# Kernel optimization log

Hardware: AMD Instinct MI355X
Metric: run time of the kernel (lower is better)

The kernel has to match this reference:

```python
import jax, jax.numpy as jnp
import numpy as np

EPS = 1e-5
B, N, K = 2, 40960, 16
D_OUT = 64
H = D_OUT // 2  # 32

PNAMES = ['mlp1_w','mlp1_b','mlp1_g','mlp1_beta','mlp1_m','mlp1_v',
          'ap1_fc_w','ap1_fc_b','ap1_mlp_w','ap1_mlp_b','ap1_g','ap1_beta','ap1_m','ap1_v',
          'mlp2_w','mlp2_b','mlp2_g','mlp2_beta','mlp2_m','mlp2_v',
          'ap2_fc_w','ap2_fc_b','ap2_mlp_w','ap2_mlp_b','ap2_g','ap2_beta','ap2_m','ap2_v']


def _conv1x1(x, w, b):
    # x: (B,C,N,K), w: (O,C) -> (B,O,N,K)
    return jnp.einsum('oc,bcnk->bonk', w, x) + b[None, :, None, None]


def _bn(x, g, beta, m, v):
    # eval-mode BatchNorm2d over channel axis 1
    scale = g / jnp.sqrt(v + EPS)
    return (x - m[None, :, None, None]) * scale[None, :, None, None] + beta[None, :, None, None]


def _gather_neighbour(pc, idx):
    # pc: (B,N,d), idx: (B,N,K) -> (B,N,K,d)
    b, n, d = pc.shape
    k = idx.shape[-1]
    flat = idx.reshape(b, n * k)
    feats = jnp.take_along_axis(pc, flat[:, :, None], axis=1)  # (B,N*K,d)
    return feats.reshape(b, n, k, d)


def _rel_pos_enc(xyz, idx):
    nbr = _gather_neighbour(xyz, idx)                       # (B,N,K,3)
    tile = jnp.broadcast_to(xyz[:, :, None, :], nbr.shape)  # (B,N,K,3)
    rel = tile - nbr
    dist = jnp.sqrt(jnp.sum(rel * rel, axis=-1, keepdims=True))
    return jnp.concatenate([dist, rel, tile, nbr], axis=-1)  # (B,N,K,10)


def _att_pool(f, fc_w, fc_b, mw, mb, g, beta, m, v):
    # f: (B,C,N,K)
    att = jax.nn.relu(_conv1x1(f, fc_w, fc_b))
    scores = jax.nn.softmax(att, axis=3)
    agg = jnp.sum(f * scores, axis=3, keepdims=True)        # (B,C,N,1)
    return jax.nn.relu(_bn(_conv1x1(agg, mw, mb), g, beta, m, v))


def _forward(xyz, feature, neigh_idx, p):
    # relative pos encoding -> (B,10,N,K)
    f_xyz = _rel_pos_enc(xyz, neigh_idx).transpose(0, 3, 1, 2)
    f_xyz = jax.nn.relu(_bn(_conv1x1(f_xyz, p['mlp1_w'], p['mlp1_b']),
                            p['mlp1_g'], p['mlp1_beta'], p['mlp1_m'], p['mlp1_v']))  # (B,H,N,K)
    f_nb = _gather_neighbour(feature[..., 0].transpose(0, 2, 1), neigh_idx).transpose(0, 3, 1, 2)  # (B,H,N,K)
    f_cat = jnp.concatenate([f_nb, f_xyz], axis=1)          # (B,D_OUT,N,K)
    f_agg = _att_pool(f_cat, p['ap1_fc_w'], p['ap1_fc_b'], p['ap1_mlp_w'], p['ap1_mlp_b'],
                      p['ap1_g'], p['ap1_beta'], p['ap1_m'], p['ap1_v'])  # (B,H,N,1)
    f_xyz = jax.nn.relu(_bn(_conv1x1(f_xyz, p['mlp2_w'], p['mlp2_b']),
                            p['mlp2_g'], p['mlp2_beta'], p['mlp2_m'], p['mlp2_v']))  # (B,H,N,K)
    f_nb = _gather_neighbour(f_agg[..., 0].transpose(0, 2, 1), neigh_idx).transpose(0, 3, 1, 2)  # (B,H,N,K)
    f_cat = jnp.concatenate([f_nb, f_xyz], axis=1)          # (B,D_OUT,N,K)
    return _att_pool(f_cat, p['ap2_fc_w'], p['ap2_fc_b'], p['ap2_mlp_w'], p['ap2_mlp_b'],
                     p['ap2_g'], p['ap2_beta'], p['ap2_m'], p['ap2_v'])  # (B,D_OUT,N,1)


def setup_inputs() -> dict:
    key = jax.random.key(0)
    ks = iter(jax.random.split(key, 64))

    def w(o, c):
        return jax.random.normal(next(ks), (o, c), jnp.float32) * float(np.sqrt(2.0 / c))

    def bias(c):
        return jax.random.normal(next(ks), (c,), jnp.float32) * 0.01

    def bnp(c):
        g = jax.random.uniform(next(ks), (c,), jnp.float32, 0.5, 1.5)
        beta = jax.random.normal(next(ks), (c,), jnp.float32) * 0.1
        m = jax.random.normal(next(ks), (c,), jnp.float32) * 0.1
        v = jax.random.uniform(next(ks), (c,), jnp.float32, 0.5, 1.5)
        return g, beta, m, v

    inp = {}
    inp['xyz'] = jax.random.normal(next(ks), (B, N, 3), jnp.float32)
    inp['feature'] = jax.random.normal(next(ks), (B, H, N, 1), jnp.float32)
    inp['mlp1_w'], inp['mlp1_b'] = w(H, 10), bias(H)
    inp['mlp1_g'], inp['mlp1_beta'], inp['mlp1_m'], inp['mlp1_v'] = bnp(H)
    inp['ap1_fc_w'], inp['ap1_fc_b'] = w(D_OUT, D_OUT), bias(D_OUT)
    inp['ap1_mlp_w'], inp['ap1_mlp_b'] = w(H, D_OUT), bias(H)
    inp['ap1_g'], inp['ap1_beta'], inp['ap1_m'], inp['ap1_v'] = bnp(H)
    inp['mlp2_w'], inp['mlp2_b'] = w(H, H), bias(H)
    inp['mlp2_g'], inp['mlp2_beta'], inp['mlp2_m'], inp['mlp2_v'] = bnp(H)
    inp['ap2_fc_w'], inp['ap2_fc_b'] = w(D_OUT, D_OUT), bias(D_OUT)
    inp['ap2_mlp_w'], inp['ap2_mlp_b'] = w(D_OUT, D_OUT), bias(D_OUT)
    inp['ap2_g'], inp['ap2_beta'], inp['ap2_m'], inp['ap2_v'] = bnp(D_OUT)
    inp['neigh_idx'] = jax.random.randint(next(ks), (B, N, K), 0, N, jnp.int64 if jax.config.jax_enable_x64 else jnp.int32)
    return inp


def reference(xyz, feature, mlp1_w, mlp1_b, mlp1_g, mlp1_beta, mlp1_m, mlp1_v,
              ap1_fc_w, ap1_fc_b, ap1_mlp_w, ap1_mlp_b, ap1_g, ap1_beta, ap1_m, ap1_v,
              mlp2_w, mlp2_b, mlp2_g, mlp2_beta, mlp2_m, mlp2_v,
              ap2_fc_w, ap2_fc_b, ap2_mlp_w, ap2_mlp_b, ap2_g, ap2_beta, ap2_m, ap2_v,
              neigh_idx):
    p = dict(zip(PNAMES, (mlp1_w, mlp1_b, mlp1_g, mlp1_beta, mlp1_m, mlp1_v,
                          ap1_fc_w, ap1_fc_b, ap1_mlp_w, ap1_mlp_b, ap1_g, ap1_beta, ap1_m, ap1_v,
                          mlp2_w, mlp2_b, mlp2_g, mlp2_beta, mlp2_m, mlp2_v,
                          ap2_fc_w, ap2_fc_b, ap2_mlp_w, ap2_mlp_b, ap2_g, ap2_beta, ap2_m, ap2_v)))
    return _forward(xyz, feature, neigh_idx, p)
```

## Files before the change

### kernel.cpp

```cpp
#include <hip/hip_runtime.h>
#include <math.h>

#define BB 2
#define NN 40960
#define KK 16

typedef float v2f __attribute__((ext_vector_type(2)));
__device__ __forceinline__ v2f fma2(v2f a, v2f b, v2f c){
  return __builtin_elementwise_fma(a, b, c);
}

template<int CTRL>
__device__ __forceinline__ float dppf(float x){
  return __int_as_float(__builtin_amdgcn_update_dpp(0, __float_as_int(x), CTRL, 0xF, 0xF, true));
}
__device__ __forceinline__ float red16_sum(float v){
  v += dppf<0xB1>(v);
  v += dppf<0x4E>(v);
  v += dppf<0x141>(v);
  v += dppf<0x140>(v);
  return v;
}

__device__ alignas(16) float g_pw1[32*10];
__device__ alignas(16) float g_pb1[32];
__device__ alignas(16) float g_pw2[32*32];
__device__ alignas(16) float g_pb2[32];
__device__ alignas(16) float g_pcw[32*64];
__device__ alignas(16) float g_pcb[32];
__device__ alignas(16) float g_pdw[64*64];
__device__ alignas(16) float g_pdb[64];

__global__ __launch_bounds__(256) void k_pre(
  const float* __restrict__ feat, float* __restrict__ feat_t,
  const float* __restrict__ w1, const float* __restrict__ b1,
  const float* __restrict__ g1, const float* __restrict__ be1, const float* __restrict__ m1, const float* __restrict__ v1,
  const float* __restrict__ w2, const float* __restrict__ b2,
  const float* __restrict__ g2, const float* __restrict__ be2, const float* __restrict__ m2, const float* __restrict__ v2,
  const float* __restrict__ cw, const float* __restrict__ cb,
  const float* __restrict__ cg, const float* __restrict__ cbe, const float* __restrict__ cm, const float* __restrict__ cv,
  const float* __restrict__ dw, const float* __restrict__ db,
  const float* __restrict__ dg, const float* __restrict__ dbe, const float* __restrict__ dm, const float* __restrict__ dv)
{
  int tid = threadIdx.x;
  int bid = blockIdx.x;
  if (bid < BB*NN/256){
    int b = bid / (NN/256);
    int n = (bid % (NN/256))*256 + tid;
    float v[32];
    #pragma unroll
    for (int h=0; h<32; ++h) v[h] = feat[((size_t)(b*32+h))*NN + n];
    float* o = feat_t + ((size_t)b*NN + n)*32;
    #pragma unroll
    for (int h=0; h<32; h+=4){ *(float4*)(o+h) = make_float4(v[h],v[h+1],v[h+2],v[h+3]); }
    return;
  }
  for (int i=tid; i<320; i+=256){ int h=i/10;
    g_pw1[i] = w1[i] * (g1[h]*rsqrtf(v1[h]+1e-5f)); }
  if (tid<32){ float s=g1[tid]*rsqrtf(v1[tid]+1e-5f);
    g_pb1[tid] = (b1[tid]-m1[tid])*s + be1[tid]; }
  for (int i=tid; i<1024; i+=256){ int h=i>>5;
    g_pw2[i] = w2[i] * (g2[h]*rsqrtf(v2[h]+1e-5f)); }
  if (tid<32){ float s=g2[tid]*rsqrtf(v2[tid]+1e-5f);
    g_pb2[tid] = (b2[tid]-m2[tid])*s + be2[tid]; }
  for (int i=tid; i<2048; i+=256){ int h=i>>6;
    g_pcw[i] = cw[i] * (cg[h]*rsqrtf(cv[h]+1e-5f)); }
  if (tid<32){ float s=cg[tid]*rsqrtf(cv[tid]+1e-5f);
    g_pcb[tid] = (cb[tid]-cm[tid])*s + cbe[tid]; }
  for (int i=tid; i<4096; i+=256){ int h=i>>6;
    g_pdw[i] = dw[i] * (dg[h]*rsqrtf(dv[h]+1e-5f)); }
  if (tid<64){ float s=dg[tid]*rsqrtf(dv[tid]+1e-5f);
    g_pdb[tid] = (db[tid]-dm[tid])*s + dbe[tid]; }
}

__global__ __launch_bounds__(256,2) void k_stage1(
  const float* __restrict__ xyz, const float* __restrict__ feat_t, const int* __restrict__ nidx,
  const float* __restrict__ fcw, const float* __restrict__ fcb,
  float* __restrict__ fagg)
{
  int tid = threadIdx.x;
  int lane = tid & 63, wvv = tid >> 6;
  int k = lane & 15, ns = lane >> 4;
  int b = blockIdx.x / (NN/16);
  int n = (blockIdx.x % (NN/16))*16 + wvv*4 + ns;
  size_t bn = (size_t)b*NN + n;
  int idxv = nidx[bn*KK + k];

  alignas(16) float fc_[64];
  const float* fb = feat_t + ((size_t)b*NN + idxv)*32;
  #pragma unroll
  for (int h=0; h<32; h+=4){ float4 x=*(const float4*)(fb+h);
    fc_[h]=x.x; fc_[h+1]=x.y; fc_[h+2]=x.z; fc_[h+3]=x.w; }

  const float* tp = xyz + bn*3;
  const float* qp = xyz + ((size_t)b*NN + idxv)*3;
  float t0=tp[0],t1=tp[1],t2=tp[2];
  float q0=qp[0],q1=qp[1],q2=qp[2];
  float r0=t0-q0,r1=t1-q1,r2=t2-q2;
  v2f e2[5] = { {sqrtf(r0*r0+r1*r1+r2*r2), r0}, {r1,r2}, {t0,t1}, {t2,q0}, {q1,q2} };

  #pragma unroll
  for (int h=0; h<32; ++h){
    const v2f* wr = (const v2f*)(g_pw1 + h*10);
    v2f acc = {g_pb1[h], 0.f};
    #pragma unroll
    for (int c=0; c<5; ++c) acc = fma2(wr[c], e2[c], acc);
    fc_[32+h] = fmaxf(acc.x+acc.y, 0.f);
  }

  const v2f* fv = (const v2f*)fc_;
  float sp4[4], sf4[4];
  #pragma unroll
  for (int ob=0; ob<64; ob+=2){
    const v2f* w0 = (const v2f*)(fcw + ob*64);
    const v2f* w1 = (const v2f*)(fcw + (ob+1)*64);
    v2f acc0 = {fcb[ob], 0.f}, acc1 = {fcb[ob+1], 0.f};
    #pragma unroll
    for (int c=0; c<32; ++c){ acc0 = fma2(w0[c], fv[c], acc0); acc1 = fma2(w1[c], fv[c], acc1); }
    float a0 = fmaxf(acc0.x+acc0.y, 0.f), a1 = fmaxf(acc1.x+acc1.y, 0.f);
    float p0 = __expf(a0), p1 = __expf(a1);
    float g0 = fc_[ob]*p0,  g1v = fc_[ob+1]*p1;
    float sp0 = red16_sum(p0), sf0 = red16_sum(g0);
    float sp1 = red16_sum(p1), sf1 = red16_sum(g1v);
    if ((ob>>2)==k){ sp4[ob&3]=sp0; sf4[ob&3]=sf0; sp4[(ob+1)&3]=sp1; sf4[(ob+1)&3]=sf1; }
  }
  v2f a01, a23;
  a01.x=__fdividef(sf4[0],sp4[0]); a01.y=__fdividef(sf4[1],sp4[1]);
  a23.x=__fdividef(sf4[2],sp4[2]); a23.y=__fdividef(sf4[3],sp4[3]);

  float o0=0.f, o1=0.f;
  #pragma unroll
  for (int h=0; h<32; ++h){
    const v2f* wr = (const v2f*)(g_pcw + h*64 + 4*k);
    v2f p2 = fma2(wr[0], a01, wr[1]*a23);
    float part = red16_sum(p2.x + p2.y);
    float val = fmaxf(part + g_pcb[h], 0.f);
    if ((h&15)==k){ if (h<16) o0=val; else o1=val; }
  }
  float* fo = fagg + bn*32;
  fo[k]=o0; fo[k+16]=o1;
}

__global__ __launch_bounds__(256,2) void k_stage2(
  const float* __restrict__ xyz, const float* __restrict__ fagg, const int* __restrict__ nidx,
  const float* __restrict__ fcw, const float* __restrict__ fcb,
  float* __restrict__ outp)
{
  int tid = threadIdx.x;
  int lane = tid & 63, wvv = tid >> 6;
  int k = lane & 15, ns = lane >> 4;
  int b = blockIdx.x / (NN/16);
  int n = (blockIdx.x % (NN/16))*16 + wvv*4 + ns;
  size_t bn = (size_t)b*NN + n;
  int idxv = nidx[bn*KK + k];

  alignas(16) float fc_[64];
  const float* fb = fagg + ((size_t)b*NN + idxv)*32;
  #pragma unroll
  for (int h=0; h<32; h+=4){ float4 x=*(const float4*)(fb+h);
    fc_[h]=x.x; fc_[h+1]=x.y; fc_[h+2]=x.z; fc_[h+3]=x.w; }

  const float* tp = xyz + bn*3;
  const float* qp = xyz + ((size_t)b*NN + idxv)*3;
  float t0=tp[0],t1=tp[1],t2=tp[2];
  float q0=qp[0],q1=qp[1],q2=qp[2];
  float r0=t0-q0,r1=t1-q1,r2=t2-q2;
  v2f e2[5] = { {sqrtf(r0*r0+r1*r1+r2*r2), r0}, {r1,r2}, {t0,t1}, {t2,q0}, {q1,q2} };

  alignas(8) float fx[32];
  #pragma unroll
  for (int h=0; h<32; ++h){
    const v2f* wr = (const v2f*)(g_pw1 + h*10);
    v2f acc = {g_pb1[h], 0.f};
    #pragma unroll
    for (int c=0; c<5; ++c) acc = fma2(wr[c], e2[c], acc);
    fx[h] = fmaxf(acc.x+acc.y, 0.f);
  }

  const v2f* fxv = (const v2f*)fx;
  #pragma unroll
  for (int h=0; h<32; ++h){
    const v2f* wr = (const v2f*)(g_pw2 + h*32);
    v2f acc = {g_pb2[h], 0.f};
    #pragma unroll
    for (int c=0; c<16; ++c) acc = fma2(wr[c], fxv[c], acc);
    fc_[32+h] = fmaxf(acc.x+acc.y, 0.f);
  }

  const v2f* fv = (const v2f*)fc_;
  float sp4[4], sf4[4];
  #pragma unroll
  for (int ob=0; ob<64; ob+=2){
    const v2f* w0 = (const v2f*)(fcw + ob*64);
    const v2f* w1 = (const v2f*)(fcw + (ob+1)*64);
    v2f acc0 = {fcb[ob], 0.f}, acc1 = {fcb[ob+1], 0.f};
    #pragma unroll
    for (int c=0; c<32; ++c){ acc0 = fma2(w0[c], fv[c], acc0); acc1 = fma2(w1[c], fv[c], acc1); }
    float a0 = fmaxf(acc0.x+acc0.y, 0.f), a1 = fmaxf(acc1.x+acc1.y, 0.f);
    float p0 = __expf(a0), p1 = __expf(a1);
    float g0 = fc_[ob]*p0,  g1v = fc_[ob+1]*p1;
    float sp0 = red16_sum(p0), sf0 = red16_sum(g0);
    float sp1 = red16_sum(p1), sf1 = red16_sum(g1v);
    if ((ob>>2)==k){ sp4[ob&3]=sp0; sf4[ob&3]=sf0; sp4[(ob+1)&3]=sp1; sf4[(ob+1)&3]=sf1; }
  }
  v2f a01, a23;
  a01.x=__fdividef(sf4[0],sp4[0]); a01.y=__fdividef(sf4[1],sp4[1]);
  a23.x=__fdividef(sf4[2],sp4[2]); a23.y=__fdividef(sf4[3],sp4[3]);

  float o4[4];
  #pragma unroll
  for (int h=0; h<64; ++h){
    const v2f* wr = (const v2f*)(g_pdw + h*64 + 4*k);
    v2f p2 = fma2(wr[0], a01, wr[1]*a23);
    float part = red16_sum(p2.x + p2.y);
    float val = fmaxf(part + g_pdb[h], 0.f);
    if ((h&15)==k) o4[h>>4] = val;
  }
  #pragma unroll
  for (int j=0; j<4; ++j)
    outp[((size_t)(b*64 + k + 16*j))*NN + n] = o4[j];
}

extern "C" void kernel_launch(void* const* d_in, const int* in_sizes, int n_in,
                              void* d_out, int out_size, void* d_ws, size_t ws_size,
                              hipStream_t stream){
  const float* xyz     = (const float*)d_in[0];
  const float* feature = (const float*)d_in[1];
  const int*   nidx    = (const int*)d_in[30];
  float* feat_t = (float*)d_ws;
  float* fagg   = feat_t + (size_t)BB*NN*32;

  k_pre<<<BB*NN/256 + 1, 256, 0, stream>>>(feature, feat_t,
    (const float*)d_in[2],(const float*)d_in[3],(const float*)d_in[4],(const float*)d_in[5],
    (const float*)d_in[6],(const float*)d_in[7],
    (const float*)d_in[16],(const float*)d_in[17],(const float*)d_in[18],(const float*)d_in[19],
    (const float*)d_in[20],(const float*)d_in[21],
    (const float*)d_in[10],(const float*)d_in[11],(const float*)d_in[12],(const float*)d_in[13],
    (const float*)d_in[14],(const float*)d_in[15],
    (const float*)d_in[24],(const float*)d_in[25],(const float*)d_in[26],(const float*)d_in[27],
    (const float*)d_in[28],(const float*)d_in[29]);
  k_stage1<<<BB*NN/16, 256, 0, stream>>>(xyz, feat_t, nidx,
    (const float*)d_in[8],(const float*)d_in[9], fagg);
  k_stage2<<<BB*NN/16, 256, 0, stream>>>(xyz, fagg, nidx,
    (const float*)d_in[22],(const float*)d_in[23], (float*)d_out);
}
```

Measured before the change: 453.3 us.

## Restructure stages so each wave loops over points with register-resident weights and LDS staging

Each wave now handles 16 points sequentially. Lane-indexed output channels keep the attention FC weights in registers, and the concatenated neighbour features are staged in LDS. This replaces the per-lane full 64x64 matvec and DPP reductions with an outer-product-style reuse across the 16 neighbours. Stage2 buffers its outputs in LDS so it can write coalesced float4 rows, and the grid shrinks to a quarter of the blocks with launch bounds raised to 3. The risks are higher register pressure from the 64-float weight arrays, serialised per-point latency inside each wave, and dependence on wave-level LDS ordering without a full barrier.

```diff
diff --git a/kernel.cpp b/kernel.cpp
--- a/kernel.cpp
+++ b/kernel.cpp
@@ -6,20 +6,14 @@
 #define KK 16
 
 typedef float v2f __attribute__((ext_vector_type(2)));
+__device__ __forceinline__ v2f mk2(float a, float b){ v2f r; r.x=a; r.y=b; return r; }
 __device__ __forceinline__ v2f fma2(v2f a, v2f b, v2f c){
   return __builtin_elementwise_fma(a, b, c);
 }
 
-template<int CTRL>
-__device__ __forceinline__ float dppf(float x){
-  return __int_as_float(__builtin_amdgcn_update_dpp(0, __float_as_int(x), CTRL, 0xF, 0xF, true));
-}
-__device__ __forceinline__ float red16_sum(float v){
-  v += dppf<0xB1>(v);
-  v += dppf<0x4E>(v);
-  v += dppf<0x141>(v);
-  v += dppf<0x140>(v);
-  return v;
+__device__ __forceinline__ void wave_sync(){
+  asm volatile("s_waitcnt lgkmcnt(0)" ::: "memory");
+  __builtin_amdgcn_sched_barrier(0);
 }
 
 __device__ alignas(16) float g_pw1[32*10];
@@ -73,152 +67,238 @@
     g_pdb[tid] = (db[tid]-dm[tid])*s + dbe[tid]; }
 }
 
-__global__ __launch_bounds__(256,2) void k_stage1(
+
+__global__ __launch_bounds__(256,3) void k_stage1(
   const float* __restrict__ xyz, const float* __restrict__ feat_t, const int* __restrict__ nidx,
   const float* __restrict__ fcw, const float* __restrict__ fcb,
   float* __restrict__ fagg)
 {
-  int tid = threadIdx.x;
-  int lane = tid & 63, wvv = tid >> 6;
-  int k = lane & 15, ns = lane >> 4;
-  int b = blockIdx.x / (NN/16);
-  int n = (blockIdx.x % (NN/16))*16 + wvv*4 + ns;
-  size_t bn = (size_t)b*NN + n;
-  int idxv = nidx[bn*KK + k];
-
-  alignas(16) float fc_[64];
-  const float* fb = feat_t + ((size_t)b*NN + idxv)*32;
-  #pragma unroll
-  for (int h=0; h<32; h+=4){ float4 x=*(const float4*)(fb+h);
-    fc_[h]=x.x; fc_[h+1]=x.y; fc_[h+2]=x.z; fc_[h+3]=x.w; }
-
-  const float* tp = xyz + bn*3;
-  const float* qp = xyz + ((size_t)b*NN + idxv)*3;
-  float t0=tp[0],t1=tp[1],t2=tp[2];
-  float q0=qp[0],q1=qp[1],q2=qp[2];
-  float r0=t0-q0,r1=t1-q1,r2=t2-q2;
-  v2f e2[5] = { {sqrtf(r0*r0+r1*r1+r2*r2), r0}, {r1,r2}, {t0,t1}, {t2,q0}, {q1,q2} };
-
-  #pragma unroll
-  for (int h=0; h<32; ++h){
-    const v2f* wr = (const v2f*)(g_pw1 + h*10);
-    v2f acc = {g_pb1[h], 0.f};
-    #pragma unroll
-    for (int c=0; c<5; ++c) acc = fma2(wr[c], e2[c], acc);
-    fc_[32+h] = fmaxf(acc.x+acc.y, 0.f);
-  }
-
-  const v2f* fv = (const v2f*)fc_;
-  float sp4[4], sf4[4];
-  #pragma unroll
-  for (int ob=0; ob<64; ob+=2){
-    const v2f* w0 = (const v2f*)(fcw + ob*64);
-    const v2f* w1 = (const v2f*)(fcw + (ob+1)*64);
-    v2f acc0 = {fcb[ob], 0.f}, acc1 = {fcb[ob+1], 0.f};
-    #pragma unroll
-    for (int c=0; c<32; ++c){ acc0 = fma2(w0[c], fv[c], acc0); acc1 = fma2(w1[c], fv[c], acc1); }
-    float a0 = fmaxf(acc0.x+acc0.y, 0.f), a1 = fmaxf(acc1.x+acc1.y, 0.f);
-    float p0 = __expf(a0), p1 = __expf(a1);
-    float g0 = fc_[ob]*p0,  g1v = fc_[ob+1]*p1;
-    float sp0 = red16_sum(p0), sf0 = red16_sum(g0);
-    float sp1 = red16_sum(p1), sf1 = red16_sum(g1v);
-    if ((ob>>2)==k){ sp4[ob&3]=sp0; sf4[ob&3]=sf0; sp4[(ob+1)&3]=sp1; sf4[(ob+1)&3]=sf1; }
-  }
-  v2f a01, a23;
-  a01.x=__fdividef(sf4[0],sp4[0]); a01.y=__fdividef(sf4[1],sp4[1]);
-  a23.x=__fdividef(sf4[2],sp4[2]); a23.y=__fdividef(sf4[3],sp4[3]);
-
-  float o0=0.f, o1=0.f;
-  #pragma unroll
-  for (int h=0; h<32; ++h){
-    const v2f* wr = (const v2f*)(g_pcw + h*64 + 4*k);
-    v2f p2 = fma2(wr[0], a01, wr[1]*a23);
-    float part = red16_sum(p2.x + p2.y);
-    float val = fmaxf(part + g_pcb[h], 0.f);
-    if ((h&15)==k){ if (h<16) o0=val; else o1=val; }
-  }
-  float* fo = fagg + bn*32;
-  fo[k]=o0; fo[k+16]=o1;
-}
-
-__global__ __launch_bounds__(256,2) void k_stage2(
+  __shared__ float s_fcat[4][16*68];
+  __shared__ float s_agg[4][64];
+  int tid = threadIdx.x, lane = tid&63, wvv = tid>>6;
+  int j = lane&15, cb = lane>>4;
+  int h_ap = lane&31, half = lane>>5;
+
+  float fcw_r[64];
+  {
+    const float4* src = (const float4*)(fcw + lane*64);
+    #pragma unroll
+    for (int c4=0;c4<16;++c4){ float4 w=src[c4];
+      fcw_r[4*c4]=w.x; fcw_r[4*c4+1]=w.y; fcw_r[4*c4+2]=w.z; fcw_r[4*c4+3]=w.w; }
+  }
+  float fcb_r = fcb[lane];
+  float pcw_r[32];
+  {
+    const float4* src = (const float4*)(g_pcw + h_ap*64 + half*32);
+    #pragma unroll
+    for (int c4=0;c4<8;++c4){ float4 w=src[c4];
+      pcw_r[4*c4]=w.x; pcw_r[4*c4+1]=w.y; pcw_r[4*c4+2]=w.z; pcw_r[4*c4+3]=w.w; }
+  }
+  float pcb_r = g_pcb[h_ap];
+
+  float* fcp = &s_fcat[wvv][0];
+  float* agp = &s_agg[wvv][0];
+  int pn0 = (blockIdx.x*4 + wvv)*16;
+  int b = (pn0 >= NN) ? 1 : 0;
+  int base = b*NN;
+
+  for (int t=0; t<16; ++t){
+    int pn = pn0 + t;
+    int idx = nidx[(size_t)pn*KK + j];
+    const float4* fbp = (const float4*)(feat_t + ((size_t)(base+idx))*32 + cb*8);
+    float4 g0 = fbp[0], g1 = fbp[1];
+
+    const float* tp = xyz + (size_t)pn*3;
+    const float* qp = xyz + (size_t)(base+idx)*3;
+    float t0=tp[0],t1=tp[1],t2=tp[2];
+    float q0=qp[0],q1=qp[1],q2=qp[2];
+    float r0=t0-q0,r1=t1-q1,r2=t2-q2;
+    v2f e2[5] = { {sqrtf(r0*r0+r1*r1+r2*r2),r0},{r1,r2},{t0,t1},{t2,q0},{q1,q2} };
+
+    float fx[32];
+    #pragma unroll
+    for (int h=0; h<32; ++h){
+      const v2f* wr = (const v2f*)(g_pw1 + h*10);
+      v2f a = mk2(g_pb1[h], 0.f);
+      #pragma unroll
+      for (int c=0;c<5;++c) a = fma2(wr[c], e2[c], a);
+      fx[h] = fmaxf(a.x+a.y, 0.f);
+    }
+    *(float4*)(fcp + j*68 + cb*8)     = g0;
+    *(float4*)(fcp + j*68 + cb*8 + 4) = g1;
+    if (lane < 16){
+      #pragma unroll
+      for (int c4=0;c4<8;++c4)
+        *(float4*)(fcp + j*68 + 32 + c4*4) =
+          make_float4(fx[4*c4],fx[4*c4+1],fx[4*c4+2],fx[4*c4+3]);
+    }
+    wave_sync();
+
+    float acc[16];
+    #pragma unroll
+    for (int j2=0;j2<16;++j2) acc[j2] = fcb_r;
+    #pragma unroll
+    for (int j2=0;j2<16;++j2){
+      const float4* fr = (const float4*)(fcp + j2*68);
+      #pragma unroll
+      for (int c4=0;c4<16;++c4){
+        float4 f = fr[c4];
+        acc[j2]=fmaf(fcw_r[4*c4+0],f.x,acc[j2]);
+        acc[j2]=fmaf(fcw_r[4*c4+1],f.y,acc[j2]);
+        acc[j2]=fmaf(fcw_r[4*c4+2],f.z,acc[j2]);
+        acc[j2]=fmaf(fcw_r[4*c4+3],f.w,acc[j2]);
+      }
+    }
+    float sp=0.f, sfp=0.f;
+    #pragma unroll
+    for (int j2=0;j2<16;++j2){ acc[j2] = __expf(fmaxf(acc[j2],0.f)); sp += acc[j2]; }
+    #pragma unroll
+    for (int j2=0;j2<16;++j2){ sfp = fmaf(fcp[j2*68 + lane], acc[j2], sfp); }
+    float aggv = __fdividef(sfp, sp);
+    agp[lane] = aggv;
+    wave_sync();
+
+    float part = 0.f;
+    const float4* ar = (const float4*)(agp + half*32);
+    #pragma unroll
+    for (int c4=0;c4<8;++c4){
+      float4 a = ar[c4];
+      part=fmaf(pcw_r[4*c4+0],a.x,part);
+      part=fmaf(pcw_r[4*c4+1],a.y,part);
+      part=fmaf(pcw_r[4*c4+2],a.z,part);
+      part=fmaf(pcw_r[4*c4+3],a.w,part);
+    }
+    part += __shfl_xor(part, 32);
+    float val = fmaxf(part + pcb_r, 0.f);
+    if (lane < 32) fagg[(size_t)pn*32 + lane] = val;
+    wave_sync();
+  }
+}
+
+__global__ __launch_bounds__(256,3) void k_stage2(
   const float* __restrict__ xyz, const float* __restrict__ fagg, const int* __restrict__ nidx,
   const float* __restrict__ fcw, const float* __restrict__ fcb,
   float* __restrict__ outp)
 {
-  int tid = threadIdx.x;
-  int lane = tid & 63, wvv = tid >> 6;
-  int k = lane & 15, ns = lane >> 4;
-  int b = blockIdx.x / (NN/16);
-  int n = (blockIdx.x % (NN/16))*16 + wvv*4 + ns;
-  size_t bn = (size_t)b*NN + n;
-  int idxv = nidx[bn*KK + k];
-
-  alignas(16) float fc_[64];
-  const float* fb = fagg + ((size_t)b*NN + idxv)*32;
+  __shared__ float s_fcat[4][16*68];
+  __shared__ float s_agg[4][64];
+  __shared__ float s_out[4][64*17];
+  __shared__ float s_w2[32*36];
+  int tid = threadIdx.x, lane = tid&63, wvv = tid>>6;
+  int j = lane&15, cb = lane>>4;
+
+  for (int i=tid; i<32*36; i+=256){ int h=i/36, c=i-h*36;
+    s_w2[i] = (c<32) ? g_pw2[h*32+c] : 0.f; }
+  __syncthreads();
+
+  float fcw_r[64];
+  {
+    const float4* src = (const float4*)(fcw + lane*64);
+    #pragma unroll
+    for (int c4=0;c4<16;++c4){ float4 w=src[c4];
+      fcw_r[4*c4]=w.x; fcw_r[4*c4+1]=w.y; fcw_r[4*c4+2]=w.z; fcw_r[4*c4+3]=w.w; }
+  }
+  float fcb_r = fcb[lane];
+  float pdb_r = g_pdb[lane];
+  float pb2_r[8];
   #pragma unroll
-  for (int h=0; h<32; h+=4){ float4 x=*(const float4*)(fb+h);
-    fc_[h]=x.x; fc_[h+1]=x.y; fc_[h+2]=x.z; fc_[h+3]=x.w; }
-
-  const float* tp = xyz + bn*3;
-  const float* qp = xyz + ((size_t)b*NN + idxv)*3;
-  float t0=tp[0],t1=tp[1],t2=tp[2];
-  float q0=qp[0],q1=qp[1],q2=qp[2];
-  float r0=t0-q0,r1=t1-q1,r2=t2-q2;
-  v2f e2[5] = { {sqrtf(r0*r0+r1*r1+r2*r2), r0}, {r1,r2}, {t0,t1}, {t2,q0}, {q1,q2} };
-
-  alignas(8) float fx[32];
-  #pragma unroll
-  for (int h=0; h<32; ++h){
-    const v2f* wr = (const v2f*)(g_pw1 + h*10);
-    v2f acc = {g_pb1[h], 0.f};
-    #pragma unroll
-    for (int c=0; c<5; ++c) acc = fma2(wr[c], e2[c], acc);
-    fx[h] = fmaxf(acc.x+acc.y, 0.f);
-  }
-
-  const v2f* fxv = (const v2f*)fx;
-  #pragma unroll
-  for (int h=0; h<32; ++h){
-    const v2f* wr = (const v2f*)(g_pw2 + h*32);
-    v2f acc = {g_pb2[h], 0.f};
-    #pragma unroll
-    for (int c=0; c<16; ++c) acc = fma2(wr[c], fxv[c], acc);
-    fc_[32+h] = fmaxf(acc.x+acc.y, 0.f);
-  }
-
-  const v2f* fv = (const v2f*)fc_;
-  float sp4[4], sf4[4];
-  #pragma unroll
-  for (int ob=0; ob<64; ob+=2){
-    const v2f* w0 = (const v2f*)(fcw + ob*64);
-    const v2f* w1 = (const v2f*)(fcw + (ob+1)*64);
-    v2f acc0 = {fcb[ob], 0.f}, acc1 = {fcb[ob+1], 0.f};
-    #pragma unroll
-    for (int c=0; c<32; ++c){ acc0 = fma2(w0[c], fv[c], acc0); acc1 = fma2(w1[c], fv[c], acc1); }
-    float a0 = fmaxf(acc0.x+acc0.y, 0.f), a1 = fmaxf(acc1.x+acc1.y, 0.f);
-    float p0 = __expf(a0), p1 = __expf(a1);
-    float g0 = fc_[ob]*p0,  g1v = fc_[ob+1]*p1;
-    float sp0 = red16_sum(p0), sf0 = red16_sum(g0);
-    float sp1 = red16_sum(p1), sf1 = red16_sum(g1v);
-    if ((ob>>2)==k){ sp4[ob&3]=sp0; sf4[ob&3]=sf0; sp4[(ob+1)&3]=sp1; sf4[(ob+1)&3]=sf1; }
-  }
-  v2f a01, a23;
-  a01.x=__fdividef(sf4[0],sp4[0]); a01.y=__fdividef(sf4[1],sp4[1]);
-  a23.x=__fdividef(sf4[2],sp4[2]); a23.y=__fdividef(sf4[3],sp4[3]);
-
-  float o4[4];
-  #pragma unroll
-  for (int h=0; h<64; ++h){
-    const v2f* wr = (const v2f*)(g_pdw + h*64 + 4*k);
-    v2f p2 = fma2(wr[0], a01, wr[1]*a23);
-    float part = red16_sum(p2.x + p2.y);
-    float val = fmaxf(part + g_pdb[h], 0.f);
-    if ((h&15)==k) o4[h>>4] = val;
-  }
-  #pragma unroll
-  for (int j=0; j<4; ++j)
-    outp[((size_t)(b*64 + k + 16*j))*NN + n] = o4[j];
+  for (int r=0;r<8;++r) pb2_r[r] = g_pb2[cb*8 + r];
+
+  float* fcp = &s_fcat[wvv][0];
+  float* agp = &s_agg[wvv][0];
+  float* sow = &s_out[wvv][0];
+  int pn0 = (blockIdx.x*4 + wvv)*16;
+  int b = (pn0 >= NN) ? 1 : 0;
+  int base = b*NN;
+
+  for (int t=0; t<16; ++t){
+    int pn = pn0 + t;
+    int idx = nidx[(size_t)pn*KK + j];
+    const float4* fbp = (const float4*)(fagg + ((size_t)(base+idx))*32 + cb*8);
+    float4 g0 = fbp[0], g1 = fbp[1];
+
+    const float* tp = xyz + (size_t)pn*3;
+    const float* qp = xyz + (size_t)(base+idx)*3;
+    float t0=tp[0],t1=tp[1],t2=tp[2];
+    float q0=qp[0],q1=qp[1],q2=qp[2];
+    float r0=t0-q0,r1=t1-q1,r2=t2-q2;
+    v2f e2[5] = { {sqrtf(r0*r0+r1*r1+r2*r2),r0},{r1,r2},{t0,t1},{t2,q0},{q1,q2} };
+
+    float fx[32];
+    #pragma unroll
+    for (int h=0; h<32; ++h){
+      const v2f* wr = (const v2f*)(g_pw1 + h*10);
+      v2f a = mk2(g_pb1[h], 0.f);
+      #pragma unroll
+      for (int c=0;c<5;++c) a = fma2(wr[c], e2[c], a);
+      fx[h] = fmaxf(a.x+a.y, 0.f);
+    }
+    float m8[8];
+    #pragma unroll
+    for (int r=0;r<8;++r){
+      const float4* wr = (const float4*)(s_w2 + (cb*8+r)*36);
+      float a = pb2_r[r];
+      #pragma unroll
+      for (int c4=0;c4<8;++c4){
+        float4 w = wr[c4];
+        a=fmaf(w.x,fx[4*c4+0],a); a=fmaf(w.y,fx[4*c4+1],a);
+        a=fmaf(w.z,fx[4*c4+2],a); a=fmaf(w.w,fx[4*c4+3],a);
+      }
+      m8[r] = fmaxf(a, 0.f);
+    }
+    *(float4*)(fcp + j*68 + cb*8)       = g0;
+    *(float4*)(fcp + j*68 + cb*8 + 4)   = g1;
+    *(float4*)(fcp + j*68 + 32 + cb*8)     = make_float4(m8[0],m8[1],m8[2],m8[3]);
+    *(float4*)(fcp + j*68 + 32 + cb*8 + 4) = make_float4(m8[4],m8[5],m8[6],m8[7]);
+    wave_sync();
+
+    float acc[16];
+    #pragma unroll
+    for (int j2=0;j2<16;++j2) acc[j2] = fcb_r;
+    #pragma unroll
+    for (int j2=0;j2<16;++j2){
+      const float4* fr = (const float4*)(fcp + j2*68);
+      #pragma unroll
+      for (int c4=0;c4<16;++c4){
+        float4 f = fr[c4];
+        acc[j2]=fmaf(fcw_r[4*c4+0],f.x,acc[j2]);
+        acc[j2]=fmaf(fcw_r[4*c4+1],f.y,acc[j2]);
+        acc[j2]=fmaf(fcw_r[4*c4+2],f.z,acc[j2]);
+        acc[j2]=fmaf(fcw_r[4*c4+3],f.w,acc[j2]);
+      }
+    }
+    float sp=0.f, sfp=0.f;
+    #pragma unroll
+    for (int j2=0;j2<16;++j2){ acc[j2] = __expf(fmaxf(acc[j2],0.f)); sp += acc[j2]; }
+    #pragma unroll
+    for (int j2=0;j2<16;++j2){ sfp = fmaf(fcp[j2*68 + lane], acc[j2], sfp); }
+    float aggv = __fdividef(sfp, sp);
+    agp[lane] = aggv;
+    wave_sync();
+
+    float part = 0.f;
+    const float4* wp = (const float4*)(g_pdw + lane*64);
+    const float4* ar = (const float4*)agp;
+    #pragma unroll
+    for (int c4=0;c4<16;++c4){
+      float4 w = wp[c4];
+      float4 a = ar[c4];
+      part=fmaf(w.x,a.x,part); part=fmaf(w.y,a.y,part);
+      part=fmaf(w.z,a.z,part); part=fmaf(w.w,a.w,part);
+    }
+    sow[lane*17 + t] = fmaxf(part + pdb_r, 0.f);
+    wave_sync();
+  }
+  {
+    int n0l = pn0 - base;
+    float* orow = outp + ((size_t)(b*64 + lane))*NN + n0l;
+    #pragma unroll
+    for (int q=0;q<4;++q){
+      float4 v = make_float4(sow[lane*17+4*q], sow[lane*17+4*q+1],
+                             sow[lane*17+4*q+2], sow[lane*17+4*q+3]);
+      *(float4*)(orow + 4*q) = v;
+    }
+  }
 }
 
 extern "C" void kernel_launch(void* const* d_in, const int* in_sizes, int n_in,
@@ -239,8 +319,8 @@
     (const float*)d_in[14],(const float*)d_in[15],
     (const float*)d_in[24],(const float*)d_in[25],(const float*)d_in[26],(const float*)d_in[27],
     (const float*)d_in[28],(const float*)d_in[29]);
-  k_stage1<<<BB*NN/16, 256, 0, stream>>>(xyz, feat_t, nidx,
+  k_stage1<<<BB*NN/64, 256, 0, stream>>>(xyz, feat_t, nidx,
     (const float*)d_in[8],(const float*)d_in[9], fagg);
-  k_stage2<<<BB*NN/16, 256, 0, stream>>>(xyz, fagg, nidx,
+  k_stage2<<<BB*NN/64, 256, 0, stream>>>(xyz, fagg, nidx,
     (const float*)d_in[22],(const float*)d_in[23], (float*)d_out);
 }
```

Result: slower. 1.413 ms (+211.7%).
